# Kernel tuning notes

Hardware: AMD Instinct MI355X
Metric: run time of the kernel (lower is better)

The kernel has to match this reference:

```python
import jax, jax.numpy as jnp
import numpy as np

# Synthetic layered DAG: 8 node-layers of width N -> 7 masked dense layers.
B = 4096        # batch
N = 2048        # nodes per DAG layer (= in_features = out_features)
DEPTH = 7       # number of weight layers (len(L) - 1)
DENSITY = 0.25  # fraction of predecessor edges present (mask sparsity)


def setup_inputs() -> dict:
    key = jax.random.key(0)
    kx, kw, km = jax.random.split(key, 3)
    x = jax.random.normal(kx, (B, N), dtype=jnp.float32)
    # Mask M: [DEPTH, N+1, N]; random 0/1 edges, last row (bias) all ones.
    m = (jax.random.uniform(km, (DEPTH, N + 1, N)) < DENSITY).astype(jnp.float32)
    M = m.at[:, -1, :].set(1.0)
    # Kaiming-uniform per column: bound = 1/sqrt(nnz_j) (torch code's init),
    # nonzero only at masked positions (W initialized to zeros elsewhere).
    nnz = jnp.maximum(M.sum(axis=1, keepdims=True), 1.0)  # [DEPTH,1,N]
    u = jax.random.uniform(kw, (DEPTH, N + 1, N), minval=-1.0, maxval=1.0)
    W = (u / jnp.sqrt(nnz)) * M
    return {"x": x, "W": W, "M": M}


def reference(x, W, M):
    # activations buffer semantics collapse to a per-layer chain because each
    # layer's preds are exactly the previous DAG layer; sinks = last layer.
    def step(acts, wm):
        w, m = wm  # [N+1, N] each
        h = jnp.concatenate(
            [acts, jnp.ones((acts.shape[0], 1), acts.dtype)], axis=1)  # [B, N+1]
        acts = jax.nn.relu(h @ (m * w))  # masked dense matmul + ReLU
        return acts, None

    out, _ = jax.lax.scan(step, x, (W, M))
    return out  # [B, N] activations of sink nodes
```

## Files before the change

### kernel.cpp

```cpp
#include <hip/hip_runtime.h>
#include <hip/hip_bf16.h>

typedef __bf16 bf16_t;
typedef __bf16 v8bf __attribute__((ext_vector_type(8)));
typedef __bf16 v4bf __attribute__((ext_vector_type(4)));
typedef float  v4f  __attribute__((ext_vector_type(4)));

#define B_ROWS 4096
#define N_COLS 2048
#define K_FULL 2049
#define KK     2048
#define DEPTH  7

#define BM 128
#define BN 128
#define BK 128
#define NKT (KK / BK)

__global__ __launch_bounds__(256) void wt_kernel(const float* __restrict__ W,
                                                 bf16_t* __restrict__ Wt) {
  __shared__ float t[64][65];
  const int l  = blockIdx.z;
  const int k0 = blockIdx.x * 64;
  const int n0 = blockIdx.y * 64;
  const int tid = threadIdx.x;
  const int r  = tid >> 4;
  const int c4 = (tid & 15) * 4;
  const float* Wl = W + (size_t)l * K_FULL * N_COLS;
#pragma unroll
  for (int it = 0; it < 4; ++it) {
    const int k = k0 + r + it * 16;
    const float4 v = *(const float4*)&Wl[(size_t)k * N_COLS + n0 + c4];
    t[c4 + 0][r + it * 16] = v.x;
    t[c4 + 1][r + it * 16] = v.y;
    t[c4 + 2][r + it * 16] = v.z;
    t[c4 + 3][r + it * 16] = v.w;
  }
  __syncthreads();
  bf16_t* Wtl = Wt + (size_t)l * N_COLS * KK;
#pragma unroll
  for (int it = 0; it < 4; ++it) {
    const int n = r + it * 16;
    v4bf o;
    o[0] = (bf16_t)t[n][c4 + 0];
    o[1] = (bf16_t)t[n][c4 + 1];
    o[2] = (bf16_t)t[n][c4 + 2];
    o[3] = (bf16_t)t[n][c4 + 3];
    *(v4bf*)&Wtl[(size_t)(n0 + n) * KK + k0 + c4] = o;
  }
}

__global__ __launch_bounds__(256) void bias_kernel(const float* __restrict__ W,
                                                   float* __restrict__ Bias) {
  const int i = (blockIdx.x * 256 + threadIdx.x) * 4;
  if (i >= DEPTH * N_COLS) return;
  const int l = i >> 11;
  const int n = i & (N_COLS - 1);
  *(float4*)&Bias[i] =
      *(const float4*)&W[(size_t)l * K_FULL * N_COLS + (size_t)KK * N_COLS + n];
}

__global__ __launch_bounds__(256) void init_kernel(const float* __restrict__ x,
                                                   bf16_t* __restrict__ A0) {
  const int c4 = (blockIdx.x * 256 + threadIdx.x) * 4;
  const int r  = blockIdx.y;
  const float4 v = *(const float4*)&x[(size_t)r * N_COLS + c4];
  v4bf o;
  o[0] = (bf16_t)v.x; o[1] = (bf16_t)v.y; o[2] = (bf16_t)v.z; o[3] = (bf16_t)v.w;
  *(v4bf*)&A0[(size_t)r * N_COLS + c4] = o;
}

__global__ __launch_bounds__(512, 4) void gemm_kernel(
    const bf16_t* __restrict__ A, const bf16_t* __restrict__ Bt,
    const float* __restrict__ bias,
    bf16_t* __restrict__ Cn, float* __restrict__ Co) {
  __shared__ __align__(16) bf16_t As[BM * BK];
  __shared__ __align__(16) bf16_t Bs[BN * BK];

  const int bid = blockIdx.x;
  const int swz = (bid & 7) * 64 + (bid >> 3);
  const int bx  = swz & 15;
  const int by  = swz >> 4;

  const int tid  = threadIdx.x;
  const int wave = tid >> 6;
  const int lane = tid & 63;
  const int m0 = by * BM;
  const int n0 = bx * BN;
  const int wm = (wave & 1) * 64;
  const int wn = (wave >> 1) * 32;
  const int quad = lane >> 4;
  const int l16  = lane & 15;

  int aoff[4], boff[4];
#pragma unroll
  for (int c = 0; c < 4; ++c) {
    const int gran = wave * 256 + c * 64 + lane;
    const int srow = gran >> 4;
    const int scol = ((gran & 15) ^ (srow & 15)) << 3;
    aoff[c] = (m0 + srow) * KK + scol;
    boff[c] = (n0 + srow) * KK + scol;
  }

  v4f acc[4][2] = {};

  for (int kt = 0; kt < NKT; ++kt) {
    const int kbase = kt * BK;
    __syncthreads();
#pragma unroll
    for (int c = 0; c < 4; ++c) {
      __builtin_amdgcn_global_load_lds(
          (const __attribute__((address_space(1))) void*)(A + aoff[c] + kbase),
          (__attribute__((address_space(3))) void*)((char*)As + wave * 4096 + c * 1024),
          16, 0, 0);
    }
#pragma unroll
    for (int c = 0; c < 4; ++c) {
      __builtin_amdgcn_global_load_lds(
          (const __attribute__((address_space(1))) void*)(Bt + boff[c] + kbase),
          (__attribute__((address_space(3))) void*)((char*)Bs + wave * 4096 + c * 1024),
          16, 0, 0);
    }
    __syncthreads();

#pragma unroll
    for (int ks = 0; ks < 4; ++ks) {
      v8bf af[4], bfr[2];
      const int kg = ks * 4 + quad;
#pragma unroll
      for (int i = 0; i < 4; ++i) {
        const int arow = wm + i * 16 + l16;
        af[i] = *(const v8bf*)&As[arow * BK + ((kg ^ (arow & 15)) << 3)];
      }
#pragma unroll
      for (int j = 0; j < 2; ++j) {
        const int brow = wn + j * 16 + l16;
        bfr[j] = *(const v8bf*)&Bs[brow * BK + ((kg ^ (brow & 15)) << 3)];
      }
#pragma unroll
      for (int i = 0; i < 4; ++i)
#pragma unroll
        for (int j = 0; j < 2; ++j)
          acc[i][j] = __builtin_amdgcn_mfma_f32_16x16x32_bf16(af[i], bfr[j],
                                                              acc[i][j], 0, 0, 0);
    }
  }

  float bv[2];
#pragma unroll
  for (int j = 0; j < 2; ++j) bv[j] = bias[n0 + wn + j * 16 + l16];
#pragma unroll
  for (int i = 0; i < 4; ++i) {
#pragma unroll
    for (int j = 0; j < 2; ++j) {
#pragma unroll
      for (int r = 0; r < 4; ++r) {
        float v = acc[i][j][r] + bv[j];
        v = v > 0.0f ? v : 0.0f;
        const int row = m0 + wm + i * 16 + quad * 4 + r;
        const int col = n0 + wn + j * 16 + l16;
        if (Co) Co[(size_t)row * N_COLS + col] = v;
        else    Cn[(size_t)row * N_COLS + col] = (bf16_t)v;
      }
    }
  }
}

extern "C" void kernel_launch(void* const* d_in, const int* in_sizes, int n_in,
                              void* d_out, int out_size, void* d_ws, size_t ws_size,
                              hipStream_t stream) {
  const float* x = (const float*)d_in[0];
  const float* W = (const float*)d_in[1];
  float* out = (float*)d_out;

  char* ws = (char*)d_ws;
  const size_t wtBytes = (size_t)DEPTH * N_COLS * KK * sizeof(bf16_t);
  const size_t aBytes  = (size_t)B_ROWS * N_COLS * sizeof(bf16_t);
  bf16_t* Wt   = (bf16_t*)ws;
  bf16_t* A0   = (bf16_t*)(ws + wtBytes);
  bf16_t* A1   = (bf16_t*)(ws + wtBytes + aBytes);
  float*  Bias = (float*)(ws + wtBytes + 2 * aBytes);

  wt_kernel<<<dim3(KK / 64, N_COLS / 64, DEPTH), 256, 0, stream>>>(W, Wt);
  bias_kernel<<<dim3((DEPTH * N_COLS / 4 + 255) / 256), 256, 0, stream>>>(W, Bias);
  init_kernel<<<dim3(N_COLS / 4 / 256, B_ROWS), 256, 0, stream>>>(x, A0);

  bf16_t* bufs[2] = {A0, A1};
  for (int l = 0; l < DEPTH; ++l) {
    const bf16_t* Ain = bufs[l & 1];
    bf16_t* Aout      = bufs[(l + 1) & 1];
    const bf16_t* Bl  = Wt + (size_t)l * N_COLS * KK;
    const float* bl   = Bias + (size_t)l * N_COLS;
    const bool last   = (l == DEPTH - 1);
    gemm_kernel<<<dim3((B_ROWS / BM) * (N_COLS / BN)), 512, 0, stream>>>(
        Ain, Bl, bl, last ? nullptr : Aout, last ? out : nullptr);
  }
}
```

Measured before the change: 478.9 us.

## Split GEMM K-dimension across wave groups with LDS reduction of partial tiles

The 8 waves are split into two K-groups of four; each wave now computes a 64x64 output subtile over half of each K tile, which raises fragment reuse per LDS read (8 fragment loads feed 16 MFMAs instead of 6 for 8). After the K loop, partial accumulators are exchanged through a reused 64KB shared buffer, summed, and each group writes half the rows. This doubles accumulator registers (64 floats per lane), which may hurt occupancy under launch_bounds(512,4), and adds a reduction phase and extra syncs at the end.

```diff
diff --git a/kernel.cpp b/kernel.cpp
--- a/kernel.cpp
+++ b/kernel.cpp
@@ -74,8 +74,9 @@
     const bf16_t* __restrict__ A, const bf16_t* __restrict__ Bt,
     const float* __restrict__ bias,
     bf16_t* __restrict__ Cn, float* __restrict__ Co) {
-  __shared__ __align__(16) bf16_t As[BM * BK];
-  __shared__ __align__(16) bf16_t Bs[BN * BK];
+  __shared__ __align__(16) char smem[65536];
+  bf16_t* As = (bf16_t*)smem;
+  bf16_t* Bs = (bf16_t*)(smem + 32768);
 
   const int bid = blockIdx.x;
   const int swz = (bid & 7) * 64 + (bid >> 3);
@@ -85,10 +86,12 @@
   const int tid  = threadIdx.x;
   const int wave = tid >> 6;
   const int lane = tid & 63;
+  const int q    = wave & 3;
+  const int kgrp = wave >> 2;
   const int m0 = by * BM;
   const int n0 = bx * BN;
-  const int wm = (wave & 1) * 64;
-  const int wn = (wave >> 1) * 32;
+  const int wm = (q & 1) * 64;
+  const int wn = (q >> 1) * 64;
   const int quad = lane >> 4;
   const int l16  = lane & 15;
 
@@ -102,7 +105,7 @@
     boff[c] = (n0 + srow) * KK + scol;
   }
 
-  v4f acc[4][2] = {};
+  v4f acc[4][4] = {};
 
   for (int kt = 0; kt < NKT; ++kt) {
     const int kbase = kt * BK;
@@ -124,40 +127,66 @@
     __syncthreads();
 
 #pragma unroll
-    for (int ks = 0; ks < 4; ++ks) {
-      v8bf af[4], bfr[2];
-      const int kg = ks * 4 + quad;
+    for (int ks = 0; ks < 2; ++ks) {
+      v8bf af[4], bfr[4];
+      const int kg = kgrp * 8 + ks * 4 + quad;
 #pragma unroll
       for (int i = 0; i < 4; ++i) {
         const int arow = wm + i * 16 + l16;
         af[i] = *(const v8bf*)&As[arow * BK + ((kg ^ (arow & 15)) << 3)];
       }
 #pragma unroll
-      for (int j = 0; j < 2; ++j) {
+      for (int j = 0; j < 4; ++j) {
         const int brow = wn + j * 16 + l16;
         bfr[j] = *(const v8bf*)&Bs[brow * BK + ((kg ^ (brow & 15)) << 3)];
       }
 #pragma unroll
       for (int i = 0; i < 4; ++i)
 #pragma unroll
-        for (int j = 0; j < 2; ++j)
+        for (int j = 0; j < 4; ++j)
           acc[i][j] = __builtin_amdgcn_mfma_f32_16x16x32_bf16(af[i], bfr[j],
                                                               acc[i][j], 0, 0, 0);
     }
   }
 
-  float bv[2];
-#pragma unroll
-  for (int j = 0; j < 2; ++j) bv[j] = bias[n0 + wn + j * 16 + l16];
-#pragma unroll
-  for (int i = 0; i < 4; ++i) {
-#pragma unroll
-    for (int j = 0; j < 2; ++j) {
+  __syncthreads();
+  float* red = (float*)smem;
+#pragma unroll
+  for (int j = 0; j < 4; ++j) {
+    if (kgrp == 0) {
+      *(v4f*)(red + q * 4096 + 2 * 1024 + j * 256 + lane * 4) = acc[2][j];
+      *(v4f*)(red + q * 4096 + 3 * 1024 + j * 256 + lane * 4) = acc[3][j];
+    } else {
+      *(v4f*)(red + q * 4096 + 0 * 1024 + j * 256 + lane * 4) = acc[0][j];
+      *(v4f*)(red + q * 4096 + 1 * 1024 + j * 256 + lane * 4) = acc[1][j];
+    }
+  }
+  __syncthreads();
+#pragma unroll
+  for (int j = 0; j < 4; ++j) {
+    if (kgrp == 0) {
+      acc[0][j] += *(const v4f*)(red + q * 4096 + 0 * 1024 + j * 256 + lane * 4);
+      acc[1][j] += *(const v4f*)(red + q * 4096 + 1 * 1024 + j * 256 + lane * 4);
+    } else {
+      acc[2][j] += *(const v4f*)(red + q * 4096 + 2 * 1024 + j * 256 + lane * 4);
+      acc[3][j] += *(const v4f*)(red + q * 4096 + 3 * 1024 + j * 256 + lane * 4);
+    }
+  }
+
+  float bv[4];
+#pragma unroll
+  for (int j = 0; j < 4; ++j) bv[j] = bias[n0 + wn + j * 16 + l16];
+  const int i0 = kgrp * 2;
+#pragma unroll
+  for (int ii = 0; ii < 2; ++ii) {
+#pragma unroll
+    for (int j = 0; j < 4; ++j) {
+      v4f a = (kgrp == 0) ? acc[ii][j] : acc[2 + ii][j];
 #pragma unroll
       for (int r = 0; r < 4; ++r) {
-        float v = acc[i][j][r] + bv[j];
+        float v = a[r] + bv[j];
         v = v > 0.0f ? v : 0.0f;
-        const int row = m0 + wm + i * 16 + quad * 4 + r;
+        const int row = m0 + wm + (i0 + ii) * 16 + quad * 4 + r;
         const int col = n0 + wn + j * 16 + l16;
         if (Co) Co[(size_t)row * N_COLS + col] = v;
         else    Cn[(size_t)row * N_COLS + col] = (bf16_t)v;
```

Result: no change. 478.0 us (-0.2%).

## Rewrite GEMM with 128x256 tiles and triple-buffered LDS ping-pong pipeline

Applied to the files above, without the earlier changes.

Enlarges the output tile to 128x256 with BK=64 and moves to a three-slot LDS ring. Global-to-LDS loads are issued two K-steps ahead and interleaved with four MFMA phases, each separated by explicit barriers and s_setprio. The aim is to hide global memory latency behind matrix math and raise the compute-to-load ratio per block. In exchange, occupancy drops to one 512-thread block per CU because of 144KB of LDS, and the hand-placed waitcnt/barrier logic must stay correct.

```diff
diff --git a/kernel.cpp b/kernel.cpp
--- a/kernel.cpp
+++ b/kernel.cpp
@@ -13,9 +13,9 @@
 #define DEPTH  7
 
 #define BM 128
-#define BN 128
-#define BK 128
-#define NKT (KK / BK)
+#define BN 256
+#define BK 64
+#define NT (KK / BK)
 
 __global__ __launch_bounds__(256) void wt_kernel(const float* __restrict__ W,
                                                  bf16_t* __restrict__ Wt) {
@@ -70,89 +70,162 @@
   *(v4bf*)&A0[(size_t)r * N_COLS + c4] = o;
 }
 
-__global__ __launch_bounds__(512, 4) void gemm_kernel(
+__global__ __launch_bounds__(512, 1) void gemm_kernel(
     const bf16_t* __restrict__ A, const bf16_t* __restrict__ Bt,
     const float* __restrict__ bias,
     bf16_t* __restrict__ Cn, float* __restrict__ Co) {
-  __shared__ __align__(16) bf16_t As[BM * BK];
-  __shared__ __align__(16) bf16_t Bs[BN * BK];
+  __shared__ __align__(16) char smem[147456];
 
   const int bid = blockIdx.x;
-  const int swz = (bid & 7) * 64 + (bid >> 3);
-  const int bx  = swz & 15;
-  const int by  = swz >> 4;
+  const int swz = (bid & 7) * 32 + (bid >> 3);
+  const int bx  = swz & 7;
+  const int by  = swz >> 3;
 
   const int tid  = threadIdx.x;
+  const int lane = tid & 63;
   const int wave = tid >> 6;
-  const int lane = tid & 63;
   const int m0 = by * BM;
   const int n0 = bx * BN;
-  const int wm = (wave & 1) * 64;
-  const int wn = (wave >> 1) * 32;
+  const int wm = (wave >> 2) * 64;
+  const int wn = (wave & 3) * 64;
   const int quad = lane >> 4;
   const int l16  = lane & 15;
 
-  int aoff[4], boff[4];
-#pragma unroll
-  for (int c = 0; c < 4; ++c) {
-    const int gran = wave * 256 + c * 64 + lane;
-    const int srow = gran >> 4;
-    const int scol = ((gran & 15) ^ (srow & 15)) << 3;
-    aoff[c] = (m0 + srow) * KK + scol;
-    boff[c] = (n0 + srow) * KK + scol;
-  }
-
-  v4f acc[4][2] = {};
-
-  for (int kt = 0; kt < NKT; ++kt) {
-    const int kbase = kt * BK;
-    __syncthreads();
-#pragma unroll
-    for (int c = 0; c < 4; ++c) {
-      __builtin_amdgcn_global_load_lds(
-          (const __attribute__((address_space(1))) void*)(A + aoff[c] + kbase),
-          (__attribute__((address_space(3))) void*)((char*)As + wave * 4096 + c * 1024),
-          16, 0, 0);
-    }
-#pragma unroll
-    for (int c = 0; c < 4; ++c) {
-      __builtin_amdgcn_global_load_lds(
-          (const __attribute__((address_space(1))) void*)(Bt + boff[c] + kbase),
-          (__attribute__((address_space(3))) void*)((char*)Bs + wave * 4096 + c * 1024),
-          16, 0, 0);
-    }
-    __syncthreads();
-
-#pragma unroll
-    for (int ks = 0; ks < 4; ++ks) {
-      v8bf af[4], bfr[2];
-      const int kg = ks * 4 + quad;
-#pragma unroll
-      for (int i = 0; i < 4; ++i) {
-        const int arow = wm + i * 16 + l16;
-        af[i] = *(const v8bf*)&As[arow * BK + ((kg ^ (arow & 15)) << 3)];
-      }
-#pragma unroll
-      for (int j = 0; j < 2; ++j) {
-        const int brow = wn + j * 16 + l16;
-        bfr[j] = *(const v8bf*)&Bs[brow * BK + ((kg ^ (brow & 15)) << 3)];
-      }
-#pragma unroll
-      for (int i = 0; i < 4; ++i)
-#pragma unroll
-        for (int j = 0; j < 2; ++j)
-          acc[i][j] = __builtin_amdgcn_mfma_f32_16x16x32_bf16(af[i], bfr[j],
-                                                              acc[i][j], 0, 0, 0);
-    }
-  }
-
-  float bv[2];
-#pragma unroll
-  for (int j = 0; j < 2; ++j) bv[j] = bias[n0 + wn + j * 16 + l16];
+  int ra[4], rb[4], X[2];
+#pragma unroll
+  for (int i = 0; i < 4; ++i) ra[i] = (wm + i * 16 + l16) * 128;
+#pragma unroll
+  for (int j = 0; j < 4; ++j) rb[j] = (wn + j * 16 + l16) * 128;
+  X[0] = ((quad)     ^ (l16 & 7)) << 4;
+  X[1] = ((4 + quad) ^ (l16 & 7)) << 4;
+
+  int ag[2], bg[4];
+#pragma unroll
+  for (int g = 0; g < 2; ++g) {
+    const int gran = g * 512 + tid, srow = gran >> 3, spos = gran & 7;
+    ag[g] = (m0 + srow) * KK + ((spos ^ (srow & 7)) << 3);
+  }
+#pragma unroll
+  for (int g = 0; g < 4; ++g) {
+    const int gran = g * 512 + tid, srow = gran >> 3, spos = gran & 7;
+    bg[g] = (n0 + srow) * KK + ((spos ^ (srow & 7)) << 3);
+  }
+
+  auto stA = [&](char* slot, int g, int kb) {
+    __builtin_amdgcn_global_load_lds(
+        (const __attribute__((address_space(1))) void*)(A + ag[g] + kb),
+        (__attribute__((address_space(3))) void*)(slot + g * 8192 + tid * 16),
+        16, 0, 0);
+  };
+  auto stB = [&](char* slot, int g, int kb) {
+    __builtin_amdgcn_global_load_lds(
+        (const __attribute__((address_space(1))) void*)(Bt + bg[g] + kb),
+        (__attribute__((address_space(3))) void*)(slot + 16384 + g * 8192 + tid * 16),
+        16, 0, 0);
+  };
+
+  v4f acc[4][4] = {};
+
+  stA(smem, 0, 0); stA(smem, 1, 0);
+  stB(smem, 0, 0); stB(smem, 1, 0); stB(smem, 2, 0); stB(smem, 3, 0);
+  stA(smem + 49152, 0, BK); stA(smem + 49152, 1, BK);
+  stB(smem + 49152, 0, BK); stB(smem + 49152, 1, BK);
+  stB(smem + 49152, 2, BK); stB(smem + 49152, 3, BK);
+  asm volatile("s_waitcnt vmcnt(6)" ::: "memory");
+  asm volatile("s_barrier" ::: "memory");
+
+  int cur = 0, nxt = 2;
+#pragma unroll 1
+  for (int kt = 0; kt < NT; ++kt) {
+    char* sA = smem + cur * 49152;
+    char* sB = sA + 16384;
+    char* dS = smem + nxt * 49152;
+    const int kb2 = (kt + 2) * BK;
+    const bool st = (kt < NT - 2);
+    v8bf afl[2][2], afh[2][2], bf0[2][2], bf1[2][2];
+
+#pragma unroll
+    for (int i = 0; i < 2; ++i)
+#pragma unroll
+      for (int ks = 0; ks < 2; ++ks) afl[i][ks] = *(const v8bf*)(sA + ra[i] + X[ks]);
+#pragma unroll
+    for (int j = 0; j < 2; ++j)
+#pragma unroll
+      for (int ks = 0; ks < 2; ++ks) bf0[j][ks] = *(const v8bf*)(sB + rb[j] + X[ks]);
+    if (st) { stA(dS, 0, kb2); stA(dS, 1, kb2); }
+    asm volatile("s_barrier" ::: "memory");
+    asm volatile("s_waitcnt lgkmcnt(0)" ::: "memory");
+    __builtin_amdgcn_s_setprio(1);
+#pragma unroll
+    for (int i = 0; i < 2; ++i)
+#pragma unroll
+      for (int j = 0; j < 2; ++j) {
+        acc[i][j] = __builtin_amdgcn_mfma_f32_16x16x32_bf16(afl[i][0], bf0[j][0], acc[i][j], 0, 0, 0);
+        acc[i][j] = __builtin_amdgcn_mfma_f32_16x16x32_bf16(afl[i][1], bf0[j][1], acc[i][j], 0, 0, 0);
+      }
+    __builtin_amdgcn_s_setprio(0);
+    asm volatile("s_barrier" ::: "memory");
+
+#pragma unroll
+    for (int j = 0; j < 2; ++j)
+#pragma unroll
+      for (int ks = 0; ks < 2; ++ks) bf1[j][ks] = *(const v8bf*)(sB + rb[2 + j] + X[ks]);
+    if (st) { stB(dS, 0, kb2); stB(dS, 1, kb2); }
+    asm volatile("s_barrier" ::: "memory");
+    asm volatile("s_waitcnt lgkmcnt(0)" ::: "memory");
+    __builtin_amdgcn_s_setprio(1);
+#pragma unroll
+    for (int i = 0; i < 2; ++i)
+#pragma unroll
+      for (int j = 0; j < 2; ++j) {
+        acc[i][2 + j] = __builtin_amdgcn_mfma_f32_16x16x32_bf16(afl[i][0], bf1[j][0], acc[i][2 + j], 0, 0, 0);
+        acc[i][2 + j] = __builtin_amdgcn_mfma_f32_16x16x32_bf16(afl[i][1], bf1[j][1], acc[i][2 + j], 0, 0, 0);
+      }
+    __builtin_amdgcn_s_setprio(0);
+    asm volatile("s_barrier" ::: "memory");
+
+#pragma unroll
+    for (int i = 0; i < 2; ++i)
+#pragma unroll
+      for (int ks = 0; ks < 2; ++ks) afh[i][ks] = *(const v8bf*)(sA + ra[2 + i] + X[ks]);
+    if (st) { stB(dS, 2, kb2); stB(dS, 3, kb2); }
+    asm volatile("s_barrier" ::: "memory");
+    asm volatile("s_waitcnt lgkmcnt(0)" ::: "memory");
+    __builtin_amdgcn_s_setprio(1);
+#pragma unroll
+    for (int i = 0; i < 2; ++i)
+#pragma unroll
+      for (int j = 0; j < 2; ++j) {
+        acc[2 + i][2 + j] = __builtin_amdgcn_mfma_f32_16x16x32_bf16(afh[i][0], bf1[j][0], acc[2 + i][2 + j], 0, 0, 0);
+        acc[2 + i][2 + j] = __builtin_amdgcn_mfma_f32_16x16x32_bf16(afh[i][1], bf1[j][1], acc[2 + i][2 + j], 0, 0, 0);
+      }
+    __builtin_amdgcn_s_setprio(0);
+    asm volatile("s_barrier" ::: "memory");
+
+    __builtin_amdgcn_s_setprio(1);
+#pragma unroll
+    for (int i = 0; i < 2; ++i)
+#pragma unroll
+      for (int j = 0; j < 2; ++j) {
+        acc[2 + i][j] = __builtin_amdgcn_mfma_f32_16x16x32_bf16(afh[i][0], bf0[j][0], acc[2 + i][j], 0, 0, 0);
+        acc[2 + i][j] = __builtin_amdgcn_mfma_f32_16x16x32_bf16(afh[i][1], bf0[j][1], acc[2 + i][j], 0, 0, 0);
+      }
+    __builtin_amdgcn_s_setprio(0);
+    if (st)                asm volatile("s_waitcnt vmcnt(6)" ::: "memory");
+    else if (kt == NT - 2) asm volatile("s_waitcnt vmcnt(0)" ::: "memory");
+    if (kt < NT - 1)       asm volatile("s_barrier" ::: "memory");
+
+    cur = (cur == 2) ? 0 : cur + 1;
+    nxt = (nxt == 2) ? 0 : nxt + 1;
+  }
+
+  float bv[4];
+#pragma unroll
+  for (int j = 0; j < 4; ++j) bv[j] = bias[n0 + wn + j * 16 + l16];
 #pragma unroll
   for (int i = 0; i < 4; ++i) {
 #pragma unroll
-    for (int j = 0; j < 2; ++j) {
+    for (int j = 0; j < 4; ++j) {
 #pragma unroll
       for (int r = 0; r < 4; ++r) {
         float v = acc[i][j][r] + bv[j];
```

Result: slower. 515.5 us (+7.6%).
